# Kernel optimization log

Measured on AMD Instinct MI355X. Metric: run time of the kernel, lower is better.

The kernel has to match this reference:

```python
import jax, jax.numpy as jnp
import numpy as np

B, N, D, H, DH, M = 4, 4096, 1024, 16, 64, 256
EPS = 1e-4


def softmax_kernel(data, P, is_query):
    # data: [b,h,n,dh], P: [m,dh]  (FAVOR+ positive softmax features)
    dn = data.shape[-1] ** -0.25
    ratio = P.shape[0] ** -0.5
    dd = jnp.einsum('bhnd,md->bhnm', dn * data, P)
    diag = (jnp.sum(data * data, axis=-1) * 0.5 * dn * dn)[..., None]  # [b,h,n,1]
    if is_query:
        mx = jnp.max(dd, axis=-1, keepdims=True)  # per-query max
    else:
        mx = jnp.max(dd)  # global max (as in torch source)
    return ratio * (jnp.exp(dd - diag - mx) + EPS)


def setup_inputs() -> dict:
    key = jax.random.key(0)
    ks = jax.random.split(key, 6)
    s = 1.0 / np.sqrt(D).astype(np.float32)
    x = jax.random.normal(ks[0], (B, N, D), jnp.float32)
    Wq = jax.random.normal(ks[1], (D, H * DH), jnp.float32) * s
    Wk = jax.random.normal(ks[2], (D, H * DH), jnp.float32) * s
    Wv = jax.random.normal(ks[3], (D, H * DH), jnp.float32) * s
    Wo = jax.random.normal(ks[4], (H * DH, D), jnp.float32) * s
    bo = jnp.zeros((D,), jnp.float32)
    P = jax.random.normal(ks[5], (M, DH), jnp.float32)  # gaussian (orthogonal) projection
    return {'x': x, 'Wq': Wq, 'Wk': Wk, 'Wv': Wv, 'Wo': Wo, 'bo': bo, 'P': P}


def reference(x, Wq, Wk, Wv, Wo, bo, P):
    b, n, _ = x.shape
    # qkv projections, split heads: b n (h d) -> b h n d
    def proj(W):
        return (x @ W).reshape(b, n, H, DH).transpose(0, 2, 1, 3)
    q, k, v = proj(Wq), proj(Wk), proj(Wv)
    qp = softmax_kernel(q, P, is_query=True)   # [b,h,n,m]
    kp = softmax_kernel(k, P, is_query=False)  # [b,h,n,m]
    # linear attention (Performer)
    k_cumsum = kp.sum(axis=-2)                                   # [b,h,m]
    D_inv = 1.0 / jnp.einsum('bhnm,bhm->bhn', qp, k_cumsum)      # [b,h,n]
    ctx = jnp.einsum('bhnm,bhne->bhme', kp, v)                   # [b,h,m,dh]
    out = jnp.einsum('bhme,bhnm,bhn->bhne', ctx, qp, D_inv)      # [b,h,n,dh]
    out = out.transpose(0, 2, 1, 3).reshape(b, n, H * DH)
    return out @ Wo + bo
```

## Files before the change

### kernel.cpp

```cpp
#include <hip/hip_runtime.h>
#include <math.h>

#define NB 4
#define NSEQ 4096
#define DM 1024
#define NHEAD 16
#define DHD 64
#define MF 256
#define ROWS 16384

#define DN 0.35355339059327373f
#define RATIO 0.0625f
#define HALF_DN2 0.0625f
#define EPSF 1.0e-4f
#define THR_DEFER 4.0f

typedef __attribute__((ext_vector_type(4))) float f32x4;
typedef __attribute__((ext_vector_type(8))) short short8;
typedef __attribute__((ext_vector_type(4))) short short4v;
typedef __attribute__((ext_vector_type(8))) __bf16 bf16x8;
typedef unsigned short ushort_t;

__device__ __forceinline__ unsigned short f2bf(float f) {
  unsigned int u = __builtin_bit_cast(unsigned int, f);
  u += 0x7FFFu + ((u >> 16) & 1u);
  return (unsigned short)(u >> 16);
}
__device__ __forceinline__ float bf2f(unsigned short h) {
  unsigned int u = ((unsigned int)h) << 16;
  return __builtin_bit_cast(float, u);
}

__device__ __forceinline__ f32x4 mfma16(short8 a, short8 b, f32x4 c) {
  return __builtin_amdgcn_mfma_f32_16x16x32_bf16(
      __builtin_bit_cast(bf16x8, a), __builtin_bit_cast(bf16x8, b), c, 0, 0, 0);
}

__device__ __forceinline__ f32x4 mfma16x16(short4v a, short4v b, f32x4 c) {
#if __has_builtin(__builtin_amdgcn_mfma_f32_16x16x16bf16_1k)
  return __builtin_amdgcn_mfma_f32_16x16x16bf16_1k(a, b, c, 0, 0, 0);
#elif __has_builtin(__builtin_amdgcn_mfma_f32_16x16x16_bf16)
  typedef __attribute__((ext_vector_type(4))) __bf16 bf16x4;
  return __builtin_amdgcn_mfma_f32_16x16x16_bf16(
      __builtin_bit_cast(bf16x4, a), __builtin_bit_cast(bf16x4, b), c, 0, 0, 0);
#else
  asm volatile("s_nop 1\n\t"
               "v_mfma_f32_16x16x16_bf16 %0, %1, %2, %0\n\t"
               "s_nop 7"
               : "+v"(c) : "v"(a), "v"(b));
  return c;
#endif
}

__device__ __forceinline__ void glds16(const void* g, void* l) {
  __builtin_amdgcn_global_load_lds(
      (const __attribute__((address_space(1))) unsigned int*)g,
      (__attribute__((address_space(3))) unsigned int*)l, 16, 0, 0);
}

__global__ __launch_bounds__(256) void wtrans(const float* __restrict__ W,
                                              ushort_t* __restrict__ Wt)
{
  __shared__ float ts[64][68];
  const int tid = threadIdx.x;
  const int k0 = blockIdx.y * 64, n0 = blockIdx.x * 64;
  const int r = tid >> 4, c4 = (tid & 15) * 4;
  #pragma unroll
  for (int i = 0; i < 4; ++i) {
    float4 v = *(const float4*)&W[(size_t)(k0 + r + i * 16) * DM + n0 + c4];
    *(float4*)&ts[r + i * 16][c4] = v;
  }
  __syncthreads();
  #pragma unroll
  for (int i = 0; i < 4; ++i) {
    const int n = r + i * 16;
    ushort4 o;
    o.x = f2bf(ts[c4 + 0][n]); o.y = f2bf(ts[c4 + 1][n]);
    o.z = f2bf(ts[c4 + 2][n]); o.w = f2bf(ts[c4 + 3][n]);
    *(ushort4*)&Wt[(size_t)(n0 + n) * DM + k0 + c4] = o;
  }
}

__global__ __launch_bounds__(256) void psplit(const float* __restrict__ P,
                                              ushort_t* __restrict__ PHI,
                                              ushort_t* __restrict__ PLO)
{
  const int i = blockIdx.x * 256 + threadIdx.x;
  const float v = P[i];
  const unsigned short h = f2bf(v);
  PHI[i] = h;
  PLO[i] = f2bf(v - bf2f(h));
}

__global__ __launch_bounds__(256) void xconv(const float* __restrict__ x,
                                             ushort_t* __restrict__ xb)
{
  const size_t i = ((size_t)blockIdx.x * 256 + threadIdx.x) * 8;
  const float4 a = *(const float4*)&x[i];
  const float4 c = *(const float4*)&x[i + 4];
  short8 o;
  o[0] = f2bf(a.x); o[1] = f2bf(a.y); o[2] = f2bf(a.z); o[3] = f2bf(a.w);
  o[4] = f2bf(c.x); o[5] = f2bf(c.y); o[6] = f2bf(c.z); o[7] = f2bf(c.w);
  *(short8*)&xb[i] = o;
}

template<int EPI>
__global__ __launch_bounds__(256) void gemm_k(const ushort_t* __restrict__ Ab,
                                              const ushort_t* __restrict__ Bt,
                                              const float* __restrict__ bias,
                                              float* __restrict__ C,
                                              ushort_t* __restrict__ VT,
                                              ushort_t* __restrict__ OHL,
                                              float* __restrict__ DIAG)
{
  constexpr int K = DM, N = DM;
  __shared__ ushort_t As[128 * 32];
  __shared__ ushort_t Bs[128 * 32];

  const int tid = threadIdx.x;
  const int l = tid & 63, w = tid >> 6;
  const int ll = l & 15, lh = l >> 4;
  const int wr = w >> 1, wc = w & 1;

  const int bid = blockIdx.x;
  const int swz = (bid & 7) * ((int)gridDim.x >> 3) + (bid >> 3);
  const int bm = swz >> 3, bn = swz & 7;
  const int row0 = bm * 128, col0 = bn * 128;

  const int pb0 = w * 128 + l, pb1 = pb0 + 64;
  const int brow0 = pb0 >> 2, bkq0 = (pb0 & 3) ^ ((brow0 >> 1) & 3);
  const int brow1 = pb1 >> 2, bkq1 = (pb1 & 3) ^ ((brow1 >> 1) & 3);
  const ushort_t* bsrc0 = Bt + (size_t)(col0 + brow0) * K + bkq0 * 8;
  const ushort_t* bsrc1 = Bt + (size_t)(col0 + brow1) * K + bkq1 * 8;
  ushort_t* bdst0 = &Bs[(size_t)(w * 128) * 8];
  ushort_t* bdst1 = &Bs[(size_t)(w * 128 + 64) * 8];

  const ushort_t* asrc0 = Ab + (size_t)(row0 + brow0) * K + bkq0 * 8;
  const ushort_t* asrc1 = Ab + (size_t)(row0 + brow1) * K + bkq1 * 8;

  int aoff[4], boff[4];
  #pragma unroll
  for (int mt = 0; mt < 4; ++mt) {
    const int r = wr * 64 + mt * 16 + ll;
    aoff[mt] = (r * 4 + (lh ^ ((r >> 1) & 3))) * 8;
  }
  #pragma unroll
  for (int nt = 0; nt < 4; ++nt) {
    const int r = wc * 64 + nt * 16 + ll;
    boff[nt] = (r * 4 + (lh ^ ((r >> 1) & 3))) * 8;
  }

  f32x4 acc[4][4];
  #pragma unroll
  for (int i = 0; i < 4; ++i)
    #pragma unroll
    for (int j = 0; j < 4; ++j) acc[i][j] = (f32x4){0.f, 0.f, 0.f, 0.f};

  for (int k0 = 0; k0 < K; k0 += 32) {
    __syncthreads();
    glds16(asrc0 + k0, &As[(size_t)(w * 128) * 8]);
    glds16(asrc1 + k0, &As[(size_t)(w * 128 + 64) * 8]);
    glds16(bsrc0 + k0, bdst0);
    glds16(bsrc1 + k0, bdst1);
    __syncthreads();

    short8 av[4], bv[4];
    #pragma unroll
    for (int mt = 0; mt < 4; ++mt) av[mt] = *(const short8*)&As[aoff[mt]];
    #pragma unroll
    for (int nt = 0; nt < 4; ++nt) bv[nt] = *(const short8*)&Bs[boff[nt]];
    #pragma unroll
    for (int mt = 0; mt < 4; ++mt)
      #pragma unroll
      for (int nt = 0; nt < 4; ++nt)
        acc[mt][nt] = mfma16(av[mt], bv[nt], acc[mt][nt]);
  }

  if constexpr (EPI == 1) {
    #pragma unroll
    for (int mt = 0; mt < 4; ++mt) {
      #pragma unroll
      for (int nt = 0; nt < 4; ++nt) {
        const int row = row0 + wr * 64 + mt * 16 + lh * 4;
        const int col = col0 + wc * 64 + nt * 16 + ll;
        const float bv_ = bias[col];
        #pragma unroll
        for (int j = 0; j < 4; ++j)
          C[(size_t)(row + j) * N + col] = acc[mt][nt][j] + bv_;
      }
    }
  } else if constexpr (EPI == 2) {
    #pragma unroll
    for (int mt = 0; mt < 4; ++mt) {
      #pragma unroll
      for (int nt = 0; nt < 4; ++nt) {
        const int rg = row0 + wr * 64 + mt * 16 + lh * 4;
        const int cg = col0 + wc * 64 + nt * 16 + ll;
        const int b = rg >> 12, n = rg & 4095;
        const int h = cg >> 6, dh = cg & 63;
        ushort4 o;
        o.x = f2bf(acc[mt][nt][0]); o.y = f2bf(acc[mt][nt][1]);
        o.z = f2bf(acc[mt][nt][2]); o.w = f2bf(acc[mt][nt][3]);
        *(ushort4*)&VT[(((size_t)b * 16 + h) * 64 + dh) * 4096 + n] = o;
      }
    }
  } else {
    const int hglob = (col0 >> 6) + wc;
    #pragma unroll
    for (int mt = 0; mt < 4; ++mt) {
      float rssq[4] = {0.f, 0.f, 0.f, 0.f};
      #pragma unroll
      for (int nt = 0; nt < 4; ++nt) {
        const int row = row0 + wr * 64 + mt * 16 + lh * 4;
        const int e = nt * 16 + ll;
        #pragma unroll
        for (int j = 0; j < 4; ++j) {
          const float v = acc[mt][nt][j];
          rssq[j] += v * v;
          const unsigned short hh = f2bf(v);
          const size_t base = ((size_t)(row + j) * 16 + hglob) * 128 + e;
          OHL[base] = hh;
          OHL[base + 64] = f2bf(v - bf2f(hh));
        }
      }
      #pragma unroll
      for (int j = 0; j < 4; ++j) {
        float s = rssq[j];
        s += __shfl_xor(s, 1, 64); s += __shfl_xor(s, 2, 64);
        s += __shfl_xor(s, 4, 64); s += __shfl_xor(s, 8, 64);
        if (ll == 0) {
          const int row = row0 + wr * 64 + mt * 16 + lh * 4 + j;
          DIAG[(((row >> 12) * 16 + hglob) << 12) + (row & 4095)] = HALF_DN2 * s;
        }
      }
    }
  }
}

__global__ __launch_bounds__(256) void kside5(const ushort_t* __restrict__ KHL,
                                              const ushort_t* __restrict__ VT,
                                              const ushort_t* __restrict__ PHI,
                                              const ushort_t* __restrict__ PLO,
                                              const float* __restrict__ DIAGK,
                                              float* __restrict__ partC,
                                              float* __restrict__ partK,
                                              float* __restrict__ mw,
                                              float* __restrict__ vsum,
                                              unsigned* __restrict__ mxp)
{
  const int tid = threadIdx.x;
  const int l = tid & 63, mg = tid >> 6;
  const int ll = l & 15, lh = l >> 4;
  const int blk = blockIdx.x;
  const int bh = blk >> 3, ck = blk & 7;
  const int b = bh >> 4, h = bh & 15;

  short8 pfh[4][2], pfl[4][2];
  #pragma unroll
  for (int mt = 0; mt < 4; ++mt)
    #pragma unroll
    for (int ks = 0; ks < 2; ++ks) {
      const size_t off = (size_t)(mg * 64 + mt * 16 + ll) * 64 + ks * 32 + lh * 8;
      pfh[mt][ks] = *(const short8*)&PHI[off];
      pfl[mt][ks] = *(const short8*)&PLO[off];
    }

  f32x4 apv[4][4];
  #pragma unroll
  for (int i = 0; i < 4; ++i)
    #pragma unroll
    for (int j = 0; j < 4; ++j) apv[i][j] = (f32x4){0.f, 0.f, 0.f, 0.f};
  float kcp[4] = {0.f, 0.f, 0.f, 0.f};
  float vs[4] = {0.f, 0.f, 0.f, 0.f};
  float m_run = -1.0e30f, tmax = -1.0e30f;

  const int n0 = ck * 512;
  const ushort_t* krow = KHL + ((size_t)(b * NSEQ + n0 + ll) * 16 + h) * 128 + lh * 8;
  const ushort_t* vrow = VT + (size_t)bh * 64 * NSEQ + n0 + lh * 4;
  const float* drow = DIAGK + bh * 4096 + n0 + lh * 4;

  short8 kh0 = *(const short8*)(krow);
  short8 kh1 = *(const short8*)(krow + 32);
  short8 kl0 = *(const short8*)(krow + 64);
  short8 kl1 = *(const short8*)(krow + 96);

  for (int it = 0; it < 32; ++it) {
    short8 nh0, nh1, nl0, nl1;
    if (it < 31) {
      const ushort_t* kp = krow + (size_t)(it + 1) * 16 * 2048;
      nh0 = *(const short8*)(kp);
      nh1 = *(const short8*)(kp + 32);
      nl0 = *(const short8*)(kp + 64);
      nl1 = *(const short8*)(kp + 96);
    }
    const float4 dg4 = *(const float4*)(drow + it * 16);
    short4v vf[4];
    #pragma unroll
    for (int dt = 0; dt < 4; ++dt)
      vf[dt] = *(const short4v*)&vrow[(size_t)(dt * 16 + ll) * NSEQ + it * 16];

    f32x4 dda[4];
    #pragma unroll
    for (int mt = 0; mt < 4; ++mt) {
      f32x4 acc = (f32x4){0.f, 0.f, 0.f, 0.f};
      acc = mfma16(kh0, pfh[mt][0], acc); acc = mfma16(kh1, pfh[mt][1], acc);
      acc = mfma16(kh0, pfl[mt][0], acc); acc = mfma16(kh1, pfl[mt][1], acc);
      acc = mfma16(kl0, pfh[mt][0], acc); acc = mfma16(kl1, pfh[mt][1], acc);
      #pragma unroll
      for (int jr = 0; jr < 4; ++jr) acc[jr] *= DN;
      dda[mt] = acc;
    }

    float pm = -1.0e30f;
    #pragma unroll
    for (int mt = 0; mt < 4; ++mt)
      #pragma unroll
      for (int jr = 0; jr < 4; ++jr) pm = fmaxf(pm, dda[mt][jr]);
    tmax = fmaxf(tmax, pm);
    if (!__all(pm <= m_run + THR_DEFER)) {
      float pw = pm;
      pw = fmaxf(pw, __shfl_xor(pw, 1, 64));  pw = fmaxf(pw, __shfl_xor(pw, 2, 64));
      pw = fmaxf(pw, __shfl_xor(pw, 4, 64));  pw = fmaxf(pw, __shfl_xor(pw, 8, 64));
      pw = fmaxf(pw, __shfl_xor(pw, 16, 64)); pw = fmaxf(pw, __shfl_xor(pw, 32, 64));
      const float sc = __expf(m_run - pw);
      #pragma unroll
      for (int mt = 0; mt < 4; ++mt) {
        kcp[mt] *= sc;
        #pragma unroll
        for (int dt = 0; dt < 4; ++dt) apv[mt][dt] *= sc;
      }
      m_run = pw;
    }

    const float dgv[4] = {dg4.x, dg4.y, dg4.z, dg4.w};
    short4v qa[4];
    #pragma unroll
    for (int mt = 0; mt < 4; ++mt) {
      short4v o;
      float s = 0.f;
      #pragma unroll
      for (int jr = 0; jr < 4; ++jr) {
        const float kv = __expf(dda[mt][jr] - dgv[jr] - m_run);
        const unsigned short ub = f2bf(kv);
        o[jr] = (short)ub;
        s += bf2f(ub);
      }
      qa[mt] = o;
      kcp[mt] += s;
    }

    if (mg == 0) {
      #pragma unroll
      for (int dt = 0; dt < 4; ++dt)
        #pragma unroll
        for (int e = 0; e < 4; ++e) vs[dt] += bf2f((ushort_t)vf[dt][e]);
    }

    #pragma unroll
    for (int dt = 0; dt < 4; ++dt)
      #pragma unroll
      for (int mt = 0; mt < 4; ++mt)
        apv[mt][dt] = mfma16x16(qa[mt], vf[dt], apv[mt][dt]);

    kh0 = nh0; kh1 = nh1; kl0 = nl0; kl1 = nl1;
  }

  #pragma unroll
  for (int mt = 0; mt < 4; ++mt) {
    float s = kcp[mt];
    s += __shfl_xor(s, 16, 64);
    s += __shfl_xor(s, 32, 64);
    if (lh == 0) partK[blk * 256 + mg * 64 + mt * 16 + ll] = s;
  }
  #pragma unroll
  for (int mt = 0; mt < 4; ++mt)
    #pragma unroll
    for (int dt = 0; dt < 4; ++dt)
      #pragma unroll
      for (int jr = 0; jr < 4; ++jr) {
        const int m = mg * 64 + mt * 16 + lh * 4 + jr;
        const int dh = dt * 16 + ll;
        partC[(size_t)blk * 16384 + (size_t)m * 64 + dh] = apv[mt][dt][jr];
      }
  if (mg == 0) {
    #pragma unroll
    for (int dt = 0; dt < 4; ++dt) {
      float s = vs[dt];
      s += __shfl_xor(s, 16, 64);
      s += __shfl_xor(s, 32, 64);
      if (lh == 0) atomicAdd(&vsum[bh * 64 + dt * 16 + ll], s);
    }
  }
  tmax = fmaxf(tmax, __shfl_xor(tmax, 1, 64));  tmax = fmaxf(tmax, __shfl_xor(tmax, 2, 64));
  tmax = fmaxf(tmax, __shfl_xor(tmax, 4, 64));  tmax = fmaxf(tmax, __shfl_xor(tmax, 8, 64));
  tmax = fmaxf(tmax, __shfl_xor(tmax, 16, 64)); tmax = fmaxf(tmax, __shfl_xor(tmax, 32, 64));
  if (l == 0) {
    atomicMax(mxp, __float_as_uint(tmax));
    mw[blk * 4 + mg] = m_run;
  }
}

__global__ __launch_bounds__(256) void combine(const float* __restrict__ partC,
                                               const float* __restrict__ partK,
                                               const float* __restrict__ mw,
                                               const float* __restrict__ vsum,
                                               const unsigned* __restrict__ mxp,
                                               float* __restrict__ KCS,
                                               ushort_t* __restrict__ CTH,
                                               ushort_t* __restrict__ CTL)
{
  const int tid = threadIdx.x;
  const int bh = blockIdx.x >> 2, mc = blockIdx.x & 3;
  const float MX = __uint_as_float(*mxp);
  float s[8];
  #pragma unroll
  for (int c = 0; c < 8; ++c)
    s[c] = RATIO * __expf(mw[(bh * 8 + c) * 4 + mc] - MX);

  __shared__ float ts[64][68];
  const int r = tid >> 4, c4 = (tid & 15) * 4;
  const float reps = RATIO * EPSF;
  const float4 v4 = *(const float4*)&vsum[bh * 64 + c4];
  #pragma unroll
  for (int i = 0; i < 4; ++i) {
    const int ml = r + i * 16;
    float4 a;
    a.x = reps * v4.x; a.y = reps * v4.y; a.z = reps * v4.z; a.w = reps * v4.w;
    #pragma unroll
    for (int c = 0; c < 8; ++c) {
      const float4 p = *(const float4*)&partC[(size_t)(bh * 8 + c) * 16384 +
                                              (size_t)(mc * 64 + ml) * 64 + c4];
      a.x += s[c] * p.x; a.y += s[c] * p.y; a.z += s[c] * p.z; a.w += s[c] * p.w;
    }
    *(float4*)&ts[ml][c4] = a;
  }
  if (tid < 64) {
    const int m = mc * 64 + tid;
    float kv = reps * 4096.0f;
    #pragma unroll
    for (int c = 0; c < 8; ++c) kv += s[c] * partK[(bh * 8 + c) * 256 + m];
    KCS[bh * 256 + m] = kv;
  }
  __syncthreads();
  #pragma unroll
  for (int i = 0; i < 4; ++i) {
    const int dh = r + i * 16;
    ushort4 oh, ol;
    #pragma unroll
    for (int k = 0; k < 4; ++k) {
      const float v = ts[c4 + k][dh];
      const unsigned short hh = f2bf(v);
      ((unsigned short*)&oh)[k] = hh;
      ((unsigned short*)&ol)[k] = f2bf(v - bf2f(hh));
    }
    const size_t o = ((size_t)bh * 64 + dh) * MF + mc * 64 + c4;
    *(ushort4*)&CTH[o] = oh;
    *(ushort4*)&CTL[o] = ol;
  }
}

__global__ __launch_bounds__(512, 2) void qside6(const ushort_t* __restrict__ QHL,
                                                 const ushort_t* __restrict__ PHI,
                                                 const ushort_t* __restrict__ PLO,
                                                 const float* __restrict__ DIAGQ,
                                                 const float* __restrict__ kcs,
                                                 const ushort_t* __restrict__ CTH,
                                                 const ushort_t* __restrict__ CTL,
                                                 ushort_t* __restrict__ attb)
{
  extern __shared__ ushort_t lds[];
  ushort_t* pst = lds;
  ushort_t* ctf = lds + 32768;
  ushort_t* kcf = lds + 65536;

  const int tid = threadIdx.x;
  const int l = tid & 63, w = tid >> 6;
  const int ll = l & 15, lh = l >> 4;
  const int bh = blockIdx.x >> 4, qt = blockIdx.x & 15;
  const int b = bh >> 4, h = bh & 15;

  #pragma unroll
  for (int i = 0; i < 8; ++i) {
    const int f = tid + i * 512;
    const int fl = f & 63, r = f >> 6;
    const int p = r & 1, ks = (r >> 1) & 1, mt = r >> 2;
    const ushort_t* src = (p ? PLO : PHI) + (mt * 16 + (fl & 15)) * 64 + ks * 32 + (fl >> 4) * 8;
    *(short8*)&pst[f * 8] = *(const short8*)src;
  }
  #pragma unroll
  for (int i = 0; i < 16; ++i) {
    const int g = tid + i * 512;
    const int gl = g & 63, r = g >> 6;
    const int dt = r & 3, r2 = r >> 2, mt = r2 & 15, p = r2 >> 4;
    const ushort_t* src = (p ? CTL : CTH) +
        ((size_t)bh * 64 + dt * 16 + (gl & 15)) * MF + mt * 16 + (gl >> 4) * 4;
    *(ushort4*)&ctf[g * 4] = *(const ushort4*)src;
  }
  #pragma unroll
  for (int i = 0; i < 2; ++i) {
    const int u = tid + i * 512;
    const int ul = u & 63, mt = u >> 6;
    const int cll = ul & 15, clh = ul >> 4;
    ushort4 o = make_ushort4(0, 0, 0, 0);
    if (cll < 2) {
      #pragma unroll
      for (int e = 0; e < 4; ++e) {
        const float kv = kcs[bh * MF + mt * 16 + clh * 4 + e];
        const unsigned short hi = f2bf(kv);
        ((ushort_t*)&o)[e] = (cll == 0) ? hi : f2bf(kv - bf2f(hi));
      }
    }
    *(ushort4*)&kcf[u * 4] = o;
  }
  __syncthreads();

  const int nloc0 = qt * 256 + w * 32;
  const int rowb0 = b * NSEQ + nloc0;

  short8 qh0[2], ql0[2], qh1[2], ql1[2];
  #pragma unroll
  for (int ks = 0; ks < 2; ++ks) {
    const size_t base = ((size_t)(rowb0 + ll) * 16 + h) * 128 + ks * 32 + lh * 8;
    qh0[ks] = *(const short8*)&QHL[base];
    ql0[ks] = *(const short8*)&QHL[base + 64];
    qh1[ks] = *(const short8*)&QHL[base + (size_t)16 * 2048];
    ql1[ks] = *(const short8*)&QHL[base + (size_t)16 * 2048 + 64];
  }
  const float dg0 = DIAGQ[bh * 4096 + nloc0 + ll];
  const float dg1 = DIAGQ[bh * 4096 + nloc0 + 16 + ll];

  f32x4 dd0[16], dd1[16];
  #pragma unroll
  for (int mt = 0; mt < 16; ++mt) {
    const short8 ph0 = *(const short8*)&pst[((mt * 2 + 0) * 2 + 0) * 512 + l * 8];
    const short8 ph1 = *(const short8*)&pst[((mt * 2 + 1) * 2 + 0) * 512 + l * 8];
    const short8 pl0 = *(const short8*)&pst[((mt * 2 + 0) * 2 + 1) * 512 + l * 8];
    const short8 pl1 = *(const short8*)&pst[((mt * 2 + 1) * 2 + 1) * 512 + l * 8];
    f32x4 a0 = (f32x4){0.f, 0.f, 0.f, 0.f};
    f32x4 a1 = (f32x4){0.f, 0.f, 0.f, 0.f};
    a0 = mfma16(ph0, qh0[0], a0); a0 = mfma16(ph1, qh0[1], a0);
    a0 = mfma16(ph0, ql0[0], a0); a0 = mfma16(ph1, ql0[1], a0);
    a0 = mfma16(pl0, qh0[0], a0); a0 = mfma16(pl1, qh0[1], a0);
    a1 = mfma16(ph0, qh1[0], a1); a1 = mfma16(ph1, qh1[1], a1);
    a1 = mfma16(ph0, ql1[0], a1); a1 = mfma16(ph1, ql1[1], a1);
    a1 = mfma16(pl0, qh1[0], a1); a1 = mfma16(pl1, qh1[1], a1);
    dd0[mt] = a0; dd1[mt] = a1;
  }

  float rm0 = -3.0e38f, rm1 = -3.0e38f;
  #pragma unroll
  for (int mt = 0; mt < 16; ++mt) {
    rm0 = fmaxf(rm0, fmaxf(fmaxf(dd0[mt][0], dd0[mt][1]), fmaxf(dd0[mt][2], dd0[mt][3])));
    rm1 = fmaxf(rm1, fmaxf(fmaxf(dd1[mt][0], dd1[mt][1]), fmaxf(dd1[mt][2], dd1[mt][3])));
  }
  rm0 = fmaxf(rm0, __shfl_xor(rm0, 16, 64)); rm0 = fmaxf(rm0, __shfl_xor(rm0, 32, 64));
  rm1 = fmaxf(rm1, __shfl_xor(rm1, 16, 64)); rm1 = fmaxf(rm1, __shfl_xor(rm1, 32, 64));
  rm0 *= DN; rm1 *= DN;

  short4v qp0[16], qp1[16];
  #pragma unroll
  for (int mt = 0; mt < 16; ++mt) {
    short4v o0, o1;
    #pragma unroll
    for (int jr = 0; jr < 4; ++jr) {
      o0[jr] = (short)f2bf(RATIO * (__expf(dd0[mt][jr] * DN - dg0 - rm0) + EPSF));
      o1[jr] = (short)f2bf(RATIO * (__expf(dd1[mt][jr] * DN - dg1 - rm1) + EPSF));
    }
    qp0[mt] = o0; qp1[mt] = o1;
  }

  f32x4 av0[4], av1[4];
  #pragma unroll
  for (int dt = 0; dt < 4; ++dt) {
    av0[dt] = (f32x4){0.f, 0.f, 0.f, 0.f};
    av1[dt] = (f32x4){0.f, 0.f, 0.f, 0.f};
  }
  f32x4 aK0 = (f32x4){0.f, 0.f, 0.f, 0.f};
  f32x4 aK1 = (f32x4){0.f, 0.f, 0.f, 0.f};
  #pragma unroll
  for (int mt = 0; mt < 16; ++mt) {
    const short4v kcv = *(const short4v*)&kcf[mt * 256 + l * 4];
    aK0 = mfma16x16(qp0[mt], kcv, aK0);
    aK1 = mfma16x16(qp1[mt], kcv, aK1);
    #pragma unroll
    for (int dt = 0; dt < 4; ++dt) {
      const short4v ch = *(const short4v*)&ctf[((0 * 16 + mt) * 4 + dt) * 256 + l * 4];
      const short4v cl = *(const short4v*)&ctf[((16 + mt) * 4 + dt) * 256 + l * 4];
      av0[dt] = mfma16x16(qp0[mt], ch, av0[dt]);
      av0[dt] = mfma16x16(qp0[mt], cl, av0[dt]);
      av1[dt] = mfma16x16(qp1[mt], ch, av1[dt]);
      av1[dt] = mfma16x16(qp1[mt], cl, av1[dt]);
    }
  }

  float di0[4], di1[4];
  #pragma unroll
  for (int jr = 0; jr < 4; ++jr) {
    const float h0 = __shfl(aK0[jr], (l & 48), 64);
    const float l0 = __shfl(aK0[jr], (l & 48) | 1, 64);
    const float h1 = __shfl(aK1[jr], (l & 48), 64);
    const float l1 = __shfl(aK1[jr], (l & 48) | 1, 64);
    di0[jr] = 1.0f / (h0 + l0);
    di1[jr] = 1.0f / (h1 + l1);
  }

  #pragma unroll
  for (int dt = 0; dt < 4; ++dt)
    #pragma unroll
    for (int jr = 0; jr < 4; ++jr) {
      const int col = h * DHD + dt * 16 + ll;
      attb[(size_t)(rowb0 + lh * 4 + jr) * DM + col] = f2bf(av0[dt][jr] * di0[jr]);
      attb[(size_t)(rowb0 + 16 + lh * 4 + jr) * DM + col] = f2bf(av1[dt][jr] * di1[jr]);
    }
}

extern "C" void kernel_launch(void* const* d_in, const int* in_sizes, int n_in,
                              void* d_out, int out_size, void* d_ws, size_t ws_size,
                              hipStream_t stream)
{
  const float* x  = (const float*)d_in[0];
  const float* Wq = (const float*)d_in[1];
  const float* Wk = (const float*)d_in[2];
  const float* Wv = (const float*)d_in[3];
  const float* Wo = (const float*)d_in[4];
  const float* bo = (const float*)d_in[5];
  const float* P  = (const float*)d_in[6];
  float* out = (float*)d_out;

  char* wp = (char*)d_ws;
  ushort_t* QHL  = (ushort_t*)(wp + 0);
  ushort_t* KHL  = (ushort_t*)(wp + 67108864);
  ushort_t* VT   = (ushort_t*)(wp + 134217728);
  ushort_t* Wqt  = (ushort_t*)(wp + 167772160);
  ushort_t* Wkt  = (ushort_t*)(wp + 169869312);
  ushort_t* Wvt  = (ushort_t*)(wp + 171966464);
  ushort_t* Wot  = (ushort_t*)(wp + 174063616);
  ushort_t* PHI  = (ushort_t*)(wp + 176160768);
  ushort_t* PLO  = (ushort_t*)(wp + 176193536);
  float*    DIAGQ= (float*)(wp + 176226304);
  float*    DIAGK= (float*)(wp + 177274880);
  float*    PARTK= (float*)(wp + 178323456);
  float*    MW   = (float*)(wp + 178847744);
  float*    VSUM = (float*)(wp + 178855936);
  unsigned* MX   = (unsigned*)(wp + 178872320);
  float*    KCS  = (float*)(wp + 178872576);
  ushort_t* CTH  = (ushort_t*)(wp + 178938112);
  ushort_t* CTL  = (ushort_t*)(wp + 181035264);
  ushort_t* ATTB = KHL;

  float*    PARTC= (float*)d_out;
  ushort_t* XB   = (ushort_t*)((char*)d_out + 33554432);

  dim3 tg(16, 16);
  wtrans<<<tg, 256, 0, stream>>>(Wq, Wqt);
  wtrans<<<tg, 256, 0, stream>>>(Wk, Wkt);
  wtrans<<<tg, 256, 0, stream>>>(Wv, Wvt);
  wtrans<<<tg, 256, 0, stream>>>(Wo, Wot);
  psplit<<<64, 256, 0, stream>>>(P, PHI, PLO);
  xconv<<<8192, 256, 0, stream>>>(x, XB);
  hipMemsetAsync(VSUM, 0, 16384 + 256, stream);

  gemm_k<3><<<1024, 256, 0, stream>>>(XB, Wqt, nullptr, nullptr, nullptr, QHL, DIAGQ);
  gemm_k<3><<<1024, 256, 0, stream>>>(XB, Wkt, nullptr, nullptr, nullptr, KHL, DIAGK);
  gemm_k<2><<<1024, 256, 0, stream>>>(XB, Wvt, nullptr, nullptr, VT, nullptr, nullptr);

  kside5<<<512, 256, 0, stream>>>(KHL, VT, PHI, PLO, DIAGK, PARTC, PARTK, MW, VSUM, MX);
  combine<<<256, 256, 0, stream>>>(PARTC, PARTK, MW, VSUM, MX, KCS, CTH, CTL);
  qside6<<<1024, 512, 139264, stream>>>(QHL, PHI, PLO, DIAGQ, KCS, CTH, CTL, ATTB);

  gemm_k<1><<<1024, 256, 0, stream>>>(ATTB, Wot, bo, out, nullptr, nullptr, nullptr);
}
```

Baseline: 427.6 us.

## Split kside over feature halves and stream query softmax with online max

The key-side kernel now splits the 256 random features into two halves per block, doubling the grid to 1024 blocks. It halves per-thread accumulators and drops the software prefetch of K, with a launch bound aimed at higher occupancy. The query-side kernel no longer holds all 16 feature tiles in registers. It computes features tile by tile with a running row max and rescales the accumulators, folding the EPS term in algebraically through precomputed column sums of ctx and k_cumsum produced by combine. This cuts register pressure and a full pass, but adds atomics, extra shuffles and possible rescale branches.

```diff
diff --git a/kernel.cpp b/kernel.cpp
--- a/kernel.cpp
+++ b/kernel.cpp
@@ -237,40 +237,41 @@
   }
 }
 
-__global__ __launch_bounds__(256) void kside5(const ushort_t* __restrict__ KHL,
-                                              const ushort_t* __restrict__ VT,
-                                              const ushort_t* __restrict__ PHI,
-                                              const ushort_t* __restrict__ PLO,
-                                              const float* __restrict__ DIAGK,
-                                              float* __restrict__ partC,
-                                              float* __restrict__ partK,
-                                              float* __restrict__ mw,
-                                              float* __restrict__ vsum,
-                                              unsigned* __restrict__ mxp)
+__global__ __launch_bounds__(256, 4) void kside6(const ushort_t* __restrict__ KHL,
+                                                 const ushort_t* __restrict__ VT,
+                                                 const ushort_t* __restrict__ PHI,
+                                                 const ushort_t* __restrict__ PLO,
+                                                 const float* __restrict__ DIAGK,
+                                                 float* __restrict__ partC,
+                                                 float* __restrict__ partK,
+                                                 float* __restrict__ mw,
+                                                 float* __restrict__ vsum,
+                                                 unsigned* __restrict__ mxp)
 {
   const int tid = threadIdx.x;
   const int l = tid & 63, mg = tid >> 6;
   const int ll = l & 15, lh = l >> 4;
   const int blk = blockIdx.x;
-  const int bh = blk >> 3, ck = blk & 7;
+  const int bh = blk >> 4, ck = (blk >> 1) & 7, mh = blk & 1;
   const int b = bh >> 4, h = bh & 15;
-
-  short8 pfh[4][2], pfl[4][2];
-  #pragma unroll
-  for (int mt = 0; mt < 4; ++mt)
+  const int mbase = mh * 128 + mg * 32;
+
+  short8 pfh[2][2], pfl[2][2];
+  #pragma unroll
+  for (int mt = 0; mt < 2; ++mt)
     #pragma unroll
     for (int ks = 0; ks < 2; ++ks) {
-      const size_t off = (size_t)(mg * 64 + mt * 16 + ll) * 64 + ks * 32 + lh * 8;
+      const size_t off = (size_t)(mbase + mt * 16 + ll) * 64 + ks * 32 + lh * 8;
       pfh[mt][ks] = *(const short8*)&PHI[off];
       pfl[mt][ks] = *(const short8*)&PLO[off];
     }
 
-  f32x4 apv[4][4];
-  #pragma unroll
-  for (int i = 0; i < 4; ++i)
+  f32x4 apv[2][4];
+  #pragma unroll
+  for (int i = 0; i < 2; ++i)
     #pragma unroll
     for (int j = 0; j < 4; ++j) apv[i][j] = (f32x4){0.f, 0.f, 0.f, 0.f};
-  float kcp[4] = {0.f, 0.f, 0.f, 0.f};
+  float kcp[2] = {0.f, 0.f};
   float vs[4] = {0.f, 0.f, 0.f, 0.f};
   float m_run = -1.0e30f, tmax = -1.0e30f;
 
@@ -279,29 +280,21 @@
   const ushort_t* vrow = VT + (size_t)bh * 64 * NSEQ + n0 + lh * 4;
   const float* drow = DIAGK + bh * 4096 + n0 + lh * 4;
 
-  short8 kh0 = *(const short8*)(krow);
-  short8 kh1 = *(const short8*)(krow + 32);
-  short8 kl0 = *(const short8*)(krow + 64);
-  short8 kl1 = *(const short8*)(krow + 96);
-
   for (int it = 0; it < 32; ++it) {
-    short8 nh0, nh1, nl0, nl1;
-    if (it < 31) {
-      const ushort_t* kp = krow + (size_t)(it + 1) * 16 * 2048;
-      nh0 = *(const short8*)(kp);
-      nh1 = *(const short8*)(kp + 32);
-      nl0 = *(const short8*)(kp + 64);
-      nl1 = *(const short8*)(kp + 96);
-    }
+    const ushort_t* kp_ = krow + (size_t)it * 16 * 2048;
+    const short8 kh0 = *(const short8*)(kp_);
+    const short8 kh1 = *(const short8*)(kp_ + 32);
+    const short8 kl0 = *(const short8*)(kp_ + 64);
+    const short8 kl1 = *(const short8*)(kp_ + 96);
     const float4 dg4 = *(const float4*)(drow + it * 16);
     short4v vf[4];
     #pragma unroll
     for (int dt = 0; dt < 4; ++dt)
       vf[dt] = *(const short4v*)&vrow[(size_t)(dt * 16 + ll) * NSEQ + it * 16];
 
-    f32x4 dda[4];
-    #pragma unroll
-    for (int mt = 0; mt < 4; ++mt) {
+    f32x4 dda[2];
+    #pragma unroll
+    for (int mt = 0; mt < 2; ++mt) {
       f32x4 acc = (f32x4){0.f, 0.f, 0.f, 0.f};
       acc = mfma16(kh0, pfh[mt][0], acc); acc = mfma16(kh1, pfh[mt][1], acc);
       acc = mfma16(kh0, pfl[mt][0], acc); acc = mfma16(kh1, pfl[mt][1], acc);
@@ -313,18 +306,18 @@
 
     float pm = -1.0e30f;
     #pragma unroll
-    for (int mt = 0; mt < 4; ++mt)
+    for (int mt = 0; mt < 2; ++mt)
       #pragma unroll
       for (int jr = 0; jr < 4; ++jr) pm = fmaxf(pm, dda[mt][jr]);
     tmax = fmaxf(tmax, pm);
     if (!__all(pm <= m_run + THR_DEFER)) {
-      float pw = pm;
+      float pw = fmaxf(pm, m_run);
       pw = fmaxf(pw, __shfl_xor(pw, 1, 64));  pw = fmaxf(pw, __shfl_xor(pw, 2, 64));
       pw = fmaxf(pw, __shfl_xor(pw, 4, 64));  pw = fmaxf(pw, __shfl_xor(pw, 8, 64));
       pw = fmaxf(pw, __shfl_xor(pw, 16, 64)); pw = fmaxf(pw, __shfl_xor(pw, 32, 64));
       const float sc = __expf(m_run - pw);
       #pragma unroll
-      for (int mt = 0; mt < 4; ++mt) {
+      for (int mt = 0; mt < 2; ++mt) {
         kcp[mt] *= sc;
         #pragma unroll
         for (int dt = 0; dt < 4; ++dt) apv[mt][dt] *= sc;
@@ -333,9 +326,9 @@
     }
 
     const float dgv[4] = {dg4.x, dg4.y, dg4.z, dg4.w};
-    short4v qa[4];
-    #pragma unroll
-    for (int mt = 0; mt < 4; ++mt) {
+    short4v qa[2];
+    #pragma unroll
+    for (int mt = 0; mt < 2; ++mt) {
       short4v o;
       float s = 0.f;
       #pragma unroll
@@ -349,7 +342,7 @@
       kcp[mt] += s;
     }
 
-    if (mg == 0) {
+    if (mh == 0 && mg == 0) {
       #pragma unroll
       for (int dt = 0; dt < 4; ++dt)
         #pragma unroll
@@ -359,30 +352,28 @@
     #pragma unroll
     for (int dt = 0; dt < 4; ++dt)
       #pragma unroll
-      for (int mt = 0; mt < 4; ++mt)
+      for (int mt = 0; mt < 2; ++mt)
         apv[mt][dt] = mfma16x16(qa[mt], vf[dt], apv[mt][dt]);
-
-    kh0 = nh0; kh1 = nh1; kl0 = nl0; kl1 = nl1;
-  }
-
-  #pragma unroll
-  for (int mt = 0; mt < 4; ++mt) {
+  }
+
+  #pragma unroll
+  for (int mt = 0; mt < 2; ++mt) {
     float s = kcp[mt];
     s += __shfl_xor(s, 16, 64);
     s += __shfl_xor(s, 32, 64);
-    if (lh == 0) partK[blk * 256 + mg * 64 + mt * 16 + ll] = s;
-  }
-  #pragma unroll
-  for (int mt = 0; mt < 4; ++mt)
+    if (lh == 0) partK[blk * 128 + mg * 32 + mt * 16 + ll] = s;
+  }
+  #pragma unroll
+  for (int mt = 0; mt < 2; ++mt)
     #pragma unroll
     for (int dt = 0; dt < 4; ++dt)
       #pragma unroll
       for (int jr = 0; jr < 4; ++jr) {
-        const int m = mg * 64 + mt * 16 + lh * 4 + jr;
+        const int ml = mg * 32 + mt * 16 + lh * 4 + jr;
         const int dh = dt * 16 + ll;
-        partC[(size_t)blk * 16384 + (size_t)m * 64 + dh] = apv[mt][dt][jr];
-      }
-  if (mg == 0) {
+        partC[(size_t)blk * 8192 + (size_t)ml * 64 + dh] = apv[mt][dt][jr];
+      }
+  if (mh == 0 && mg == 0) {
     #pragma unroll
     for (int dt = 0; dt < 4; ++dt) {
       float s = vs[dt];
@@ -400,22 +391,29 @@
   }
 }
 
-__global__ __launch_bounds__(256) void combine(const float* __restrict__ partC,
-                                               const float* __restrict__ partK,
-                                               const float* __restrict__ mw,
-                                               const float* __restrict__ vsum,
-                                               const unsigned* __restrict__ mxp,
-                                               float* __restrict__ KCS,
-                                               ushort_t* __restrict__ CTH,
-                                               ushort_t* __restrict__ CTL)
+__global__ __launch_bounds__(256) void combine2(const float* __restrict__ partC,
+                                                const float* __restrict__ partK,
+                                                const float* __restrict__ mw,
+                                                const float* __restrict__ vsum,
+                                                const unsigned* __restrict__ mxp,
+                                                float* __restrict__ KCS,
+                                                ushort_t* __restrict__ CTH,
+                                                ushort_t* __restrict__ CTL,
+                                                float* __restrict__ CTSUM,
+                                                float* __restrict__ KCSSUM)
 {
   const int tid = threadIdx.x;
   const int bh = blockIdx.x >> 2, mc = blockIdx.x & 3;
+  const int mh = mc >> 1;
   const float MX = __uint_as_float(*mxp);
-  float s[8];
-  #pragma unroll
-  for (int c = 0; c < 8; ++c)
-    s[c] = RATIO * __expf(mw[(bh * 8 + c) * 4 + mc] - MX);
+  float s[8][2];
+  #pragma unroll
+  for (int c = 0; c < 8; ++c) {
+    const int blkc = bh * 16 + c * 2 + mh;
+    #pragma unroll
+    for (int g = 0; g < 2; ++g)
+      s[c][g] = RATIO * __expf(mw[blkc * 4 + (mc & 1) * 2 + g] - MX);
+  }
 
   __shared__ float ts[64][68];
   const int r = tid >> 4, c4 = (tid & 15) * 4;
@@ -424,31 +422,43 @@
   #pragma unroll
   for (int i = 0; i < 4; ++i) {
     const int ml = r + i * 16;
+    const int g = ml >> 5;
+    const int mloc = (mc & 1) * 64 + ml;
     float4 a;
     a.x = reps * v4.x; a.y = reps * v4.y; a.z = reps * v4.z; a.w = reps * v4.w;
     #pragma unroll
     for (int c = 0; c < 8; ++c) {
-      const float4 p = *(const float4*)&partC[(size_t)(bh * 8 + c) * 16384 +
-                                              (size_t)(mc * 64 + ml) * 64 + c4];
-      a.x += s[c] * p.x; a.y += s[c] * p.y; a.z += s[c] * p.z; a.w += s[c] * p.w;
+      const size_t blkc = bh * 16 + c * 2 + mh;
+      const float4 p = *(const float4*)&partC[blkc * 8192 + (size_t)mloc * 64 + c4];
+      a.x += s[c][g] * p.x; a.y += s[c][g] * p.y;
+      a.z += s[c][g] * p.z; a.w += s[c][g] * p.w;
     }
     *(float4*)&ts[ml][c4] = a;
   }
   if (tid < 64) {
     const int m = mc * 64 + tid;
+    const int g = tid >> 5;
+    const int mloc = (mc & 1) * 64 + tid;
     float kv = reps * 4096.0f;
     #pragma unroll
-    for (int c = 0; c < 8; ++c) kv += s[c] * partK[(bh * 8 + c) * 256 + m];
+    for (int c = 0; c < 8; ++c)
+      kv += s[c][g] * partK[(bh * 16 + c * 2 + mh) * 128 + mloc];
     KCS[bh * 256 + m] = kv;
+    float ks = kv;
+    #pragma unroll
+    for (int off = 1; off < 64; off <<= 1) ks += __shfl_xor(ks, off, 64);
+    if (tid == 0) atomicAdd(&KCSSUM[bh], ks);
   }
   __syncthreads();
   #pragma unroll
   for (int i = 0; i < 4; ++i) {
     const int dh = r + i * 16;
     ushort4 oh, ol;
+    float csum = 0.f;
     #pragma unroll
     for (int k = 0; k < 4; ++k) {
       const float v = ts[c4 + k][dh];
+      csum += v;
       const unsigned short hh = f2bf(v);
       ((unsigned short*)&oh)[k] = hh;
       ((unsigned short*)&ol)[k] = f2bf(v - bf2f(hh));
@@ -456,22 +466,28 @@
     const size_t o = ((size_t)bh * 64 + dh) * MF + mc * 64 + c4;
     *(ushort4*)&CTH[o] = oh;
     *(ushort4*)&CTL[o] = ol;
-  }
-}
-
-__global__ __launch_bounds__(512, 2) void qside6(const ushort_t* __restrict__ QHL,
+    csum += __shfl_xor(csum, 1, 64); csum += __shfl_xor(csum, 2, 64);
+    csum += __shfl_xor(csum, 4, 64); csum += __shfl_xor(csum, 8, 64);
+    if ((tid & 15) == 0) atomicAdd(&CTSUM[bh * 64 + dh], csum);
+  }
+}
+
+__global__ __launch_bounds__(512, 2) void qside7(const ushort_t* __restrict__ QHL,
                                                  const ushort_t* __restrict__ PHI,
                                                  const ushort_t* __restrict__ PLO,
                                                  const float* __restrict__ DIAGQ,
                                                  const float* __restrict__ kcs,
                                                  const ushort_t* __restrict__ CTH,
                                                  const ushort_t* __restrict__ CTL,
+                                                 const float* __restrict__ CTSUM,
+                                                 const float* __restrict__ KCSSUM,
                                                  ushort_t* __restrict__ attb)
 {
   extern __shared__ ushort_t lds[];
   ushort_t* pst = lds;
   ushort_t* ctf = lds + 32768;
   ushort_t* kcf = lds + 65536;
+  float* ctsum_s = (float*)(lds + 69632);
 
   const int tid = threadIdx.x;
   const int l = tid & 63, w = tid >> 6;
@@ -512,7 +528,8 @@
     }
     *(ushort4*)&kcf[u * 4] = o;
   }
-  __syncthreads();
+  if (tid < 64) ctsum_s[tid] = CTSUM[bh * 64 + tid];
+  const float kcss = KCSSUM[bh];
 
   const int nloc0 = qt * 256 + w * 32;
   const int rowb0 = b * NSEQ + nloc0;
@@ -529,8 +546,18 @@
   const float dg0 = DIAGQ[bh * 4096 + nloc0 + ll];
   const float dg1 = DIAGQ[bh * 4096 + nloc0 + 16 + ll];
 
-  f32x4 dd0[16], dd1[16];
-  #pragma unroll
+  __syncthreads();
+
+  f32x4 av0[4], av1[4];
+  #pragma unroll
+  for (int dt = 0; dt < 4; ++dt) {
+    av0[dt] = (f32x4){0.f, 0.f, 0.f, 0.f};
+    av1[dt] = (f32x4){0.f, 0.f, 0.f, 0.f};
+  }
+  f32x4 aK0 = (f32x4){0.f, 0.f, 0.f, 0.f};
+  f32x4 aK1 = (f32x4){0.f, 0.f, 0.f, 0.f};
+  float m0 = -1.0e30f, m1 = -1.0e30f, t0 = -1.0e30f, t1 = -1.0e30f;
+
   for (int mt = 0; mt < 16; ++mt) {
     const short8 ph0 = *(const short8*)&pst[((mt * 2 + 0) * 2 + 0) * 512 + l * 8];
     const short8 ph1 = *(const short8*)&pst[((mt * 2 + 1) * 2 + 0) * 512 + l * 8];
@@ -544,74 +571,80 @@
     a1 = mfma16(ph0, qh1[0], a1); a1 = mfma16(ph1, qh1[1], a1);
     a1 = mfma16(ph0, ql1[0], a1); a1 = mfma16(ph1, ql1[1], a1);
     a1 = mfma16(pl0, qh1[0], a1); a1 = mfma16(pl1, qh1[1], a1);
-    dd0[mt] = a0; dd1[mt] = a1;
-  }
-
-  float rm0 = -3.0e38f, rm1 = -3.0e38f;
-  #pragma unroll
-  for (int mt = 0; mt < 16; ++mt) {
-    rm0 = fmaxf(rm0, fmaxf(fmaxf(dd0[mt][0], dd0[mt][1]), fmaxf(dd0[mt][2], dd0[mt][3])));
-    rm1 = fmaxf(rm1, fmaxf(fmaxf(dd1[mt][0], dd1[mt][1]), fmaxf(dd1[mt][2], dd1[mt][3])));
-  }
-  rm0 = fmaxf(rm0, __shfl_xor(rm0, 16, 64)); rm0 = fmaxf(rm0, __shfl_xor(rm0, 32, 64));
-  rm1 = fmaxf(rm1, __shfl_xor(rm1, 16, 64)); rm1 = fmaxf(rm1, __shfl_xor(rm1, 32, 64));
-  rm0 *= DN; rm1 *= DN;
-
-  short4v qp0[16], qp1[16];
-  #pragma unroll
-  for (int mt = 0; mt < 16; ++mt) {
-    short4v o0, o1;
+    #pragma unroll
+    for (int jr = 0; jr < 4; ++jr) { a0[jr] *= DN; a1[jr] *= DN; }
+
+    const float pm0 = fmaxf(fmaxf(a0[0], a0[1]), fmaxf(a0[2], a0[3]));
+    const float pm1 = fmaxf(fmaxf(a1[0], a1[1]), fmaxf(a1[2], a1[3]));
+    t0 = fmaxf(t0, pm0);
+    t1 = fmaxf(t1, pm1);
+    if (!__all((pm0 <= m0 + THR_DEFER) && (pm1 <= m1 + THR_DEFER))) {
+      float pw0 = fmaxf(pm0, m0), pw1 = fmaxf(pm1, m1);
+      pw0 = fmaxf(pw0, __shfl_xor(pw0, 16, 64)); pw0 = fmaxf(pw0, __shfl_xor(pw0, 32, 64));
+      pw1 = fmaxf(pw1, __shfl_xor(pw1, 16, 64)); pw1 = fmaxf(pw1, __shfl_xor(pw1, 32, 64));
+      const float sc0l = __expf(m0 - pw0);
+      const float sc1l = __expf(m1 - pw1);
+      m0 = pw0; m1 = pw1;
+      #pragma unroll
+      for (int jr = 0; jr < 4; ++jr) {
+        const int src = (l & 48) | (lh * 4 + jr);
+        const float s0 = __shfl(sc0l, src, 64);
+        const float s1 = __shfl(sc1l, src, 64);
+        #pragma unroll
+        for (int dt = 0; dt < 4; ++dt) { av0[dt][jr] *= s0; av1[dt][jr] *= s1; }
+        aK0[jr] *= s0; aK1[jr] *= s1;
+      }
+    }
+
+    short4v qp0, qp1;
     #pragma unroll
     for (int jr = 0; jr < 4; ++jr) {
-      o0[jr] = (short)f2bf(RATIO * (__expf(dd0[mt][jr] * DN - dg0 - rm0) + EPSF));
-      o1[jr] = (short)f2bf(RATIO * (__expf(dd1[mt][jr] * DN - dg1 - rm1) + EPSF));
-    }
-    qp0[mt] = o0; qp1[mt] = o1;
-  }
-
-  f32x4 av0[4], av1[4];
+      qp0[jr] = (short)f2bf(__expf(a0[jr] - dg0 - m0));
+      qp1[jr] = (short)f2bf(__expf(a1[jr] - dg1 - m1));
+    }
+    const short4v kcv = *(const short4v*)&kcf[mt * 256 + l * 4];
+    aK0 = mfma16x16(qp0, kcv, aK0);
+    aK1 = mfma16x16(qp1, kcv, aK1);
+    #pragma unroll
+    for (int dt = 0; dt < 4; ++dt) {
+      const short4v ch = *(const short4v*)&ctf[(mt * 4 + dt) * 256 + l * 4];
+      const short4v cl = *(const short4v*)&ctf[((16 + mt) * 4 + dt) * 256 + l * 4];
+      av0[dt] = mfma16x16(qp0, ch, av0[dt]);
+      av0[dt] = mfma16x16(qp0, cl, av0[dt]);
+      av1[dt] = mfma16x16(qp1, ch, av1[dt]);
+      av1[dt] = mfma16x16(qp1, cl, av1[dt]);
+    }
+  }
+
+  t0 = fmaxf(t0, __shfl_xor(t0, 16, 64)); t0 = fmaxf(t0, __shfl_xor(t0, 32, 64));
+  t1 = fmaxf(t1, __shfl_xor(t1, 16, 64)); t1 = fmaxf(t1, __shfl_xor(t1, 32, 64));
+
+  float e0s[4], e1s[4], di0[4], di1[4];
+  #pragma unroll
+  for (int jr = 0; jr < 4; ++jr) {
+    const int src = (l & 48) | (lh * 4 + jr);
+    e0s[jr] = __expf(__shfl(m0, src, 64) - __shfl(t0, src, 64));
+    e1s[jr] = __expf(__shfl(m1, src, 64) - __shfl(t1, src, 64));
+    const float h0 = __shfl(aK0[jr], (l & 48), 64);
+    const float lo0 = __shfl(aK0[jr], (l & 48) | 1, 64);
+    const float h1 = __shfl(aK1[jr], (l & 48), 64);
+    const float lo1 = __shfl(aK1[jr], (l & 48) | 1, 64);
+    di0[jr] = 1.0f / (e0s[jr] * (h0 + lo0) + EPSF * kcss);
+    di1[jr] = 1.0f / (e1s[jr] * (h1 + lo1) + EPSF * kcss);
+  }
+
   #pragma unroll
   for (int dt = 0; dt < 4; ++dt) {
-    av0[dt] = (f32x4){0.f, 0.f, 0.f, 0.f};
-    av1[dt] = (f32x4){0.f, 0.f, 0.f, 0.f};
-  }
-  f32x4 aK0 = (f32x4){0.f, 0.f, 0.f, 0.f};
-  f32x4 aK1 = (f32x4){0.f, 0.f, 0.f, 0.f};
-  #pragma unroll
-  for (int mt = 0; mt < 16; ++mt) {
-    const short4v kcv = *(const short4v*)&kcf[mt * 256 + l * 4];
-    aK0 = mfma16x16(qp0[mt], kcv, aK0);
-    aK1 = mfma16x16(qp1[mt], kcv, aK1);
-    #pragma unroll
-    for (int dt = 0; dt < 4; ++dt) {
-      const short4v ch = *(const short4v*)&ctf[((0 * 16 + mt) * 4 + dt) * 256 + l * 4];
-      const short4v cl = *(const short4v*)&ctf[((16 + mt) * 4 + dt) * 256 + l * 4];
-      av0[dt] = mfma16x16(qp0[mt], ch, av0[dt]);
-      av0[dt] = mfma16x16(qp0[mt], cl, av0[dt]);
-      av1[dt] = mfma16x16(qp1[mt], ch, av1[dt]);
-      av1[dt] = mfma16x16(qp1[mt], cl, av1[dt]);
-    }
-  }
-
-  float di0[4], di1[4];
-  #pragma unroll
-  for (int jr = 0; jr < 4; ++jr) {
-    const float h0 = __shfl(aK0[jr], (l & 48), 64);
-    const float l0 = __shfl(aK0[jr], (l & 48) | 1, 64);
-    const float h1 = __shfl(aK1[jr], (l & 48), 64);
-    const float l1 = __shfl(aK1[jr], (l & 48) | 1, 64);
-    di0[jr] = 1.0f / (h0 + l0);
-    di1[jr] = 1.0f / (h1 + l1);
-  }
-
-  #pragma unroll
-  for (int dt = 0; dt < 4; ++dt)
+    const int col = h * DHD + dt * 16 + ll;
+    const float cts = EPSF * ctsum_s[dt * 16 + ll];
     #pragma unroll
     for (int jr = 0; jr < 4; ++jr) {
-      const int col = h * DHD + dt * 16 + ll;
-      attb[(size_t)(rowb0 + lh * 4 + jr) * DM + col] = f2bf(av0[dt][jr] * di0[jr]);
-      attb[(size_t)(rowb0 + 16 + lh * 4 + jr) * DM + col] = f2bf(av1[dt][jr] * di1[jr]);
-    }
+      const float num0 = e0s[jr] * av0[dt][jr] + cts;
+      const float num1 = e1s[jr] * av1[dt][jr] + cts;
+      attb[(size_t)(rowb0 + lh * 4 + jr) * DM + col] = f2bf(num0 * di0[jr]);
+      attb[(size_t)(rowb0 + 16 + lh * 4 + jr) * DM + col] = f2bf(num1 * di1[jr]);
+    }
+  }
 }
 
 extern "C" void kernel_launch(void* const* d_in, const int* in_sizes, int n_in,
@@ -628,28 +661,30 @@
   float* out = (float*)d_out;
 
   char* wp = (char*)d_ws;
-  ushort_t* QHL  = (ushort_t*)(wp + 0);
-  ushort_t* KHL  = (ushort_t*)(wp + 67108864);
-  ushort_t* VT   = (ushort_t*)(wp + 134217728);
-  ushort_t* Wqt  = (ushort_t*)(wp + 167772160);
-  ushort_t* Wkt  = (ushort_t*)(wp + 169869312);
-  ushort_t* Wvt  = (ushort_t*)(wp + 171966464);
-  ushort_t* Wot  = (ushort_t*)(wp + 174063616);
-  ushort_t* PHI  = (ushort_t*)(wp + 176160768);
-  ushort_t* PLO  = (ushort_t*)(wp + 176193536);
-  float*    DIAGQ= (float*)(wp + 176226304);
-  float*    DIAGK= (float*)(wp + 177274880);
-  float*    PARTK= (float*)(wp + 178323456);
-  float*    MW   = (float*)(wp + 178847744);
-  float*    VSUM = (float*)(wp + 178855936);
-  unsigned* MX   = (unsigned*)(wp + 178872320);
-  float*    KCS  = (float*)(wp + 178872576);
-  ushort_t* CTH  = (ushort_t*)(wp + 178938112);
-  ushort_t* CTL  = (ushort_t*)(wp + 181035264);
-  ushort_t* ATTB = KHL;
-
-  float*    PARTC= (float*)d_out;
-  ushort_t* XB   = (ushort_t*)((char*)d_out + 33554432);
+  ushort_t* QHL   = (ushort_t*)(wp + 0);
+  ushort_t* KHL   = (ushort_t*)(wp + 67108864);
+  ushort_t* VT    = (ushort_t*)(wp + 134217728);
+  ushort_t* Wqt   = (ushort_t*)(wp + 167772160);
+  ushort_t* Wkt   = (ushort_t*)(wp + 169869312);
+  ushort_t* Wvt   = (ushort_t*)(wp + 171966464);
+  ushort_t* Wot   = (ushort_t*)(wp + 174063616);
+  ushort_t* PHI   = (ushort_t*)(wp + 176160768);
+  ushort_t* PLO   = (ushort_t*)(wp + 176193536);
+  float*    DIAGQ = (float*)(wp + 176226304);
+  float*    DIAGK = (float*)(wp + 177274880);
+  float*    PARTK = (float*)(wp + 178323456);
+  float*    MW    = (float*)(wp + 178847744);
+  float*    VSUM  = (float*)(wp + 178864128);
+  unsigned* MX    = (unsigned*)(wp + 178880512);
+  float*    CTSUM = (float*)(wp + 178880768);
+  float*    KCSSUM= (float*)(wp + 178897152);
+  float*    KCS   = (float*)(wp + 178897408);
+  ushort_t* CTH   = (ushort_t*)(wp + 178962944);
+  ushort_t* CTL   = (ushort_t*)(wp + 181060096);
+  ushort_t* ATTB  = KHL;
+
+  float*    PARTC = (float*)d_out;
+  ushort_t* XB    = (ushort_t*)((char*)d_out + 33554432);
 
   dim3 tg(16, 16);
   wtrans<<<tg, 256, 0, stream>>>(Wq, Wqt);
@@ -658,15 +693,15 @@
   wtrans<<<tg, 256, 0, stream>>>(Wo, Wot);
   psplit<<<64, 256, 0, stream>>>(P, PHI, PLO);
   xconv<<<8192, 256, 0, stream>>>(x, XB);
-  hipMemsetAsync(VSUM, 0, 16384 + 256, stream);
+  hipMemsetAsync(VSUM, 0, 33280, stream);
 
   gemm_k<3><<<1024, 256, 0, stream>>>(XB, Wqt, nullptr, nullptr, nullptr, QHL, DIAGQ);
   gemm_k<3><<<1024, 256, 0, stream>>>(XB, Wkt, nullptr, nullptr, nullptr, KHL, DIAGK);
   gemm_k<2><<<1024, 256, 0, stream>>>(XB, Wvt, nullptr, nullptr, VT, nullptr, nullptr);
 
-  kside5<<<512, 256, 0, stream>>>(KHL, VT, PHI, PLO, DIAGK, PARTC, PARTK, MW, VSUM, MX);
-  combine<<<256, 256, 0, stream>>>(PARTC, PARTK, MW, VSUM, MX, KCS, CTH, CTL);
-  qside6<<<1024, 512, 139264, stream>>>(QHL, PHI, PLO, DIAGQ, KCS, CTH, CTL, ATTB);
+  kside6<<<1024, 256, 0, stream>>>(KHL, VT, PHI, PLO, DIAGK, PARTC, PARTK, MW, VSUM, MX);
+  combine2<<<256, 256, 0, stream>>>(PARTC, PARTK, MW, VSUM, MX, KCS, CTH, CTL, CTSUM, KCSSUM);
+  qside7<<<1024, 512, 139520, stream>>>(QHL, PHI, PLO, DIAGQ, KCS, CTH, CTL, CTSUM, KCSSUM, ATTB);
 
   gemm_k<1><<<1024, 256, 0, stream>>>(ATTB, Wot, bo, out, nullptr, nullptr, nullptr);
 }
```

Result: slower. 489.6 us (+14.5%).
